# Kernel optimization log

Hardware: AMD Instinct MI355X
Metric: run time of the kernel (lower is better)

The kernel has to match this reference:

```python
import jax, jax.numpy as jnp
import numpy as np

KH = KW = 3
STRIDE = 1
ITERATIONS = 2
EPS = 1e-7


def _squash(s):
    # squash along last axis (capsule dim)
    sn = jnp.sum(s * s, axis=-1, keepdims=True)
    return (sn / (1.0 + sn)) * s / jnp.sqrt(sn + EPS)


def setup_inputs() -> dict:
    key = jax.random.key(0)
    k1, k2 = jax.random.split(key)
    x = jax.random.normal(k1, (4, 14, 14, 32, 8), dtype=jnp.float32)
    # W: [1,1,1,filters_out, caps_per_patch=3*3*32, dims_out=16, dims_in=8], stddev=0.1 init
    W = 0.1 * jax.random.normal(k2, (1, 1, 1, 32, 288, 16, 8), dtype=jnp.float32)
    return {"x": x, "W": W}


def reference(x, W):
    B, H, Wd, Fin, Din = x.shape
    Ho = (H - KH) // STRIDE + 1
    Wo = (Wd - KW) // STRIDE + 1
    # Patch extraction, channel order (kh, kw, Fin) to match tf.image.extract_patches
    patches = jnp.stack(
        [x[:, i:i + Ho * STRIDE:STRIDE, j:j + Wo * STRIDE:STRIDE]
         for i in range(KH) for j in range(KW)],
        axis=3,
    )  # [B,Ho,Wo,KH*KW,Fin,Din]
    patches = patches.reshape(B, Ho, Wo, KH * KW * Fin, Din)  # [B,Ho,Wo,C,Di]

    Wm = W[0, 0, 0]  # [F, C, Do, Di]
    F, C, Do, _ = Wm.shape
    # predictions[b,h,w,f,c,o] = sum_i W[f,c,o,i] * patches[b,h,w,c,i]
    preds = jnp.einsum('fcoi,bhwci->bhwfco', Wm, patches)

    logits = jnp.zeros((B, Ho, Wo, F, C), dtype=preds.dtype)
    outputs = jnp.zeros((B, Ho, Wo, F, Do), dtype=preds.dtype)
    for _ in range(ITERATIONS):
        # agreement = predictions^T @ outputs over the dims_out axis
        agreement = jnp.einsum('bhwfco,bhwfo->bhwfc', preds, outputs)
        logits = logits + agreement
        # NOTE: original code softmaxes over axis=3 (the filters_out axis)
        cc = jax.nn.softmax(logits, axis=3)  # [B,Ho,Wo,F,C]
        centroids = jnp.sum(cc[..., None] * preds, axis=4)  # [B,Ho,Wo,F,Do]
        outputs = _squash(centroids)
    return outputs
```

## Files before the change

kernel.cpp:

```cpp
#include <hip/hip_runtime.h>

#define NB   4
#define H_IN 14
#define W_IN 14
#define FIN  32
#define DI   8
#define F    32
#define C    288
#define DO   16
#define HO   12
#define WO   12
#define NPOS (NB*HO*WO)
#define EPS  1e-7f

#define CH   16
#define CC   (C/CH)
#define GP   8
#define GRID (CH*(NPOS/GP))

#define KTOT (C*DI)
#define KPAD 2312

#define W2H_BYTES  ((size_t)F*C*DO*DI*2)
#define WH_BYTES   ((size_t)F*C*DO*DI*2)
#define PH_BYTES   ((size_t)NPOS*KTOT*2)
#define PART_BYTES ((size_t)CH*NPOS*F*DO*4)
#define OUT1_BYTES ((size_t)NPOS*F*DO*4)

#define CVT_W2H 576
#define CVT_WH  576
#define CVT_PH  648
#define CVT_GRID (CVT_W2H + CVT_WH + CVT_PH)

typedef _Float16 h2 __attribute__((ext_vector_type(2)));
typedef _Float16 h8v __attribute__((ext_vector_type(8)));
typedef float    f4v __attribute__((ext_vector_type(4)));

__device__ __forceinline__ unsigned int pack2(float a, float b) {
    h2 v; v.x = (_Float16)a; v.y = (_Float16)b;
    return __builtin_bit_cast(unsigned int, v);
}

__device__ __forceinline__ float dot8h(const uint4 w, const uint4 v, float acc) {
#if __has_builtin(__builtin_amdgcn_fdot2)
    acc = __builtin_amdgcn_fdot2(__builtin_bit_cast(h2, w.x), __builtin_bit_cast(h2, v.x), acc, false);
    acc = __builtin_amdgcn_fdot2(__builtin_bit_cast(h2, w.y), __builtin_bit_cast(h2, v.y), acc, false);
    acc = __builtin_amdgcn_fdot2(__builtin_bit_cast(h2, w.z), __builtin_bit_cast(h2, v.z), acc, false);
    acc = __builtin_amdgcn_fdot2(__builtin_bit_cast(h2, w.w), __builtin_bit_cast(h2, v.w), acc, false);
#else
    const h2 w0 = __builtin_bit_cast(h2, w.x), v0 = __builtin_bit_cast(h2, v.x);
    const h2 w1 = __builtin_bit_cast(h2, w.y), v1 = __builtin_bit_cast(h2, v.y);
    const h2 w2 = __builtin_bit_cast(h2, w.z), v2 = __builtin_bit_cast(h2, v.z);
    const h2 w3 = __builtin_bit_cast(h2, w.w), v3 = __builtin_bit_cast(h2, v.w);
    acc += (float)w0.x*(float)v0.x + (float)w0.y*(float)v0.y
         + (float)w1.x*(float)v1.x + (float)w1.y*(float)v1.y
         + (float)w2.x*(float)v2.x + (float)w2.y*(float)v2.y
         + (float)w3.x*(float)v3.x + (float)w3.y*(float)v3.y;
#endif
    return acc;
}

__device__ __forceinline__ int xbase_of(int pos) {
    const int b = pos/(HO*WO), rem = pos%(HO*WO), ho = rem/WO, wo = rem%WO;
    return ((b*H_IN + ho)*W_IN + wo)*FIN*DI;
}

__device__ __forceinline__ int coff_of(int c) {
    const int slab = c >> 5, fin = c & 31;
    const int kh = slab/3, kw = slab%3;
    return (kh*W_IN + kw)*FIN*DI + fin*DI;
}

__global__ __launch_bounds__(256) void kernConv(const float* __restrict__ Wt,
                                                const float* __restrict__ x,
                                                unsigned short* __restrict__ W2h,
                                                unsigned short* __restrict__ Wh,
                                                unsigned short* __restrict__ Ph) {
    const int b = blockIdx.x;
    if (b < CVT_W2H) {
        const int idx = b*256 + threadIdx.x;
        const float* src = Wt + (size_t)idx*8;
        const float4 a = *(const float4*)src;
        const float4 bb = *(const float4*)(src + 4);
        uint4 r;
        r.x = pack2(a.x, a.y);   r.y = pack2(a.z, a.w);
        r.z = pack2(bb.x, bb.y); r.w = pack2(bb.z, bb.w);
        const int o = idx & 15;
        const int c = (idx >> 4) % C;
        const int f = idx / (C*DO);
        ((uint4*)W2h)[(size_t)(c*DO + o)*F + f] = r;
    } else if (b < CVT_W2H + CVT_WH) {
        const int idx = (b - CVT_W2H)*256 + threadIdx.x;
        const float* src = Wt + (size_t)idx*8;
        const float4 a = *(const float4*)src;
        const float4 bb = *(const float4*)(src + 4);
        uint4 r;
        r.x = pack2(a.x, a.y);   r.y = pack2(a.z, a.w);
        r.z = pack2(bb.x, bb.y); r.w = pack2(bb.z, bb.w);
        ((uint4*)Wh)[idx] = r;
    } else {
        const int pc = (b - CVT_W2H - CVT_WH)*256 + threadIdx.x;
        const int pos = pc / C, c = pc % C;
        const float* src = x + xbase_of(pos) + coff_of(c);
        const float4 a = *(const float4*)src;
        const float4 bb = *(const float4*)(src + 4);
        uint4 r;
        r.x = pack2(a.x, a.y);   r.y = pack2(a.z, a.w);
        r.z = pack2(bb.x, bb.y); r.w = pack2(bb.z, bb.w);
        ((uint4*)Ph)[pc] = r;
    }
}

__global__ __launch_bounds__(256) void kernM1(const unsigned short* __restrict__ Ph,
                                              const unsigned short* __restrict__ Wh,
                                              float* __restrict__ out1)
{
    __shared__ unsigned short As[16][KPAD];

    const int tid  = threadIdx.x;
    const int lane = tid & 63;
    const int wv   = tid >> 6;
    const int pt   = blockIdx.x >> 3;
    const int fg   = blockIdx.x & 7;
    const int f    = wv*8 + fg;
    const int pos0 = pt*16;
    const int n    = lane & 15, q = lane >> 4;

    #pragma unroll
    for (int r = 0; r < 18; ++r) {
        const int linear = r*256 + tid;
        const int row = linear / 288, col8 = linear % 288;
        const uint4 v = *(const uint4*)(Ph + (size_t)(pos0 + row)*KTOT + col8*8);
        *(uint4*)&As[row][col8*8] = v;
    }
    __syncthreads();

    const unsigned short* pa = &As[n][q*8];
    const unsigned short* pb = Wh + ((size_t)(f*C + q)*DO + n)*DI;

    f4v acc0 = {0.f,0.f,0.f,0.f}, acc1 = {0.f,0.f,0.f,0.f};
    #pragma unroll 4
    for (int s = 0; s < KTOT/32; s += 2) {
        const h8v a0 = *(const h8v*)(pa + s*32);
        const h8v b0 = *(const h8v*)(pb + (size_t)s*4*DO*DI);
        const h8v a1 = *(const h8v*)(pa + (s+1)*32);
        const h8v b1 = *(const h8v*)(pb + (size_t)(s+1)*4*DO*DI);
        acc0 = __builtin_amdgcn_mfma_f32_16x16x32_f16(a0, b0, acc0, 0, 0, 0);
        acc1 = __builtin_amdgcn_mfma_f32_16x16x32_f16(a1, b1, acc1, 0, 0, 0);
    }

    #pragma unroll
    for (int r = 0; r < 4; ++r) {
        const float v = (acc0[r] + acc1[r]) * (1.f/32.f);
        float sq = v*v;
        sq += __shfl_xor(sq, 1);
        sq += __shfl_xor(sq, 2);
        sq += __shfl_xor(sq, 4);
        sq += __shfl_xor(sq, 8);
        const float sc = (sq/(1.f + sq)) * rsqrtf(sq + EPS);
        out1[(size_t)(pos0 + q*4 + r)*512 + f*DO + n] = v * sc;
    }
}

__global__ __launch_bounds__(256) void kern2n(const unsigned short* __restrict__ Ph,
                                              const unsigned short* __restrict__ W2h,
                                              const float* __restrict__ out1,
                                              float* __restrict__ part2)
{
    __shared__ float red[2][4][GP][32];
    __shared__ float ccs[2][GP][32];

    const int tid = threadIdx.x;
    const int f  = tid & 31;
    const int og = tid >> 5;
    const int o0 = 2*og, o1 = o0 + 1;
    const int wv = tid >> 6;
    const int half = (tid >> 5) & 1;
    const int ch = blockIdx.x & (CH-1);
    const int pg = blockIdx.x >> 4;

    int poff[GP];
    #pragma unroll
    for (int p = 0; p < GP; ++p) poff[p] = (pg*GP + p)*KTOT;

    float u0[GP], u1[GP];
    #pragma unroll
    for (int p = 0; p < GP; ++p) {
        const float* up = out1 + (size_t)(pg*GP + p)*512 + f*DO;
        u0[p] = up[o0];
        u1[p] = up[o1];
    }

    const uint4* W2h4 = (const uint4*)W2h;
    const int c0 = ch*CC;

    float acc0[GP], acc1[GP];
    #pragma unroll
    for (int p = 0; p < GP; ++p) { acc0[p] = 0.f; acc1[p] = 0.f; }

    #pragma unroll 1
    for (int cl = 0; cl < CC; ++cl) {
        const int c = c0 + cl;
        const int buf = cl & 1;
        const uint4 w0 = W2h4[(size_t)(c*DO + o0)*F + f];
        const uint4 w1 = W2h4[(size_t)(c*DO + o1)*F + f];

        float pred0[GP], pred1[GP];
        #pragma unroll
        for (int p = 0; p < GP; ++p) {
            const uint4 xv = *(const uint4*)(Ph + poff[p] + c*DI);
            pred0[p] = dot8h(w0, xv, 0.f);
            pred1[p] = dot8h(w1, xv, 0.f);
        }

        #pragma unroll
        for (int p = 0; p < GP; ++p) {
            float ap = pred0[p]*u0[p] + pred1[p]*u1[p];
            ap += __shfl_xor(ap, 32);
            if (half == 0) red[buf][wv][p][f] = ap;
        }
        __syncthreads();

        {
            const int p2 = tid >> 5, f2 = tid & 31;
            const float agr = red[buf][0][p2][f2] + red[buf][1][p2][f2]
                            + red[buf][2][p2][f2] + red[buf][3][p2][f2];
            float m = agr;
            m = fmaxf(m, __shfl_xor(m, 1));
            m = fmaxf(m, __shfl_xor(m, 2));
            m = fmaxf(m, __shfl_xor(m, 4));
            m = fmaxf(m, __shfl_xor(m, 8));
            m = fmaxf(m, __shfl_xor(m, 16));
            const float e = __expf(agr - m);
            float s = e;
            s += __shfl_xor(s, 1);
            s += __shfl_xor(s, 2);
            s += __shfl_xor(s, 4);
            s += __shfl_xor(s, 8);
            s += __shfl_xor(s, 16);
            ccs[buf][p2][f2] = e / s;
        }
        __syncthreads();

        #pragma unroll
        for (int p = 0; p < GP; ++p) {
            const float cv = ccs[buf][p][f];
            acc0[p] += cv*pred0[p];
            acc1[p] += cv*pred1[p];
        }
    }

    #pragma unroll
    for (int p = 0; p < GP; ++p) {
        const size_t base = ((size_t)(ch*NPOS + pg*GP + p))*DO;
        part2[(base + o0)*F + f] = acc0[p];
        part2[(base + o1)*F + f] = acc1[p];
    }
}

__global__ __launch_bounds__(256) void kern3(const float* __restrict__ part2,
                                             float* __restrict__ out)
{
    const int tid = threadIdx.x;
    const int f = tid & 31, p = tid >> 5;
    const int pos = blockIdx.x*8 + p;

    float cent[DO];
    #pragma unroll
    for (int o = 0; o < DO; ++o) cent[o] = 0.f;
    #pragma unroll 1
    for (int k = 0; k < CH; ++k) {
        const float* s = part2 + (size_t)(k*NPOS + pos)*512 + f;
        #pragma unroll
        for (int o = 0; o < DO; ++o) cent[o] += s[o*F];
    }
    float sn = 0.f;
    #pragma unroll
    for (int o = 0; o < DO; ++o) sn += cent[o]*cent[o];
    const float sc = (sn/(1.f + sn)) * rsqrtf(sn + EPS);
    float* dst = out + ((size_t)pos*F + f)*DO;
    #pragma unroll
    for (int o = 0; o < DO; ++o) dst[o] = cent[o]*sc;
}

__device__ __forceinline__ float dot8(const float4* __restrict__ w,
                                      const float4 p0, const float4 p1) {
    float4 a = w[0], b = w[1];
    return a.x*p0.x + a.y*p0.y + a.z*p0.z + a.w*p0.w
         + b.x*p1.x + b.y*p1.y + b.z*p1.z + b.w*p1.w;
}

__global__ __launch_bounds__(256) void capsule_kernel_f32(
    const float* __restrict__ x, const float* __restrict__ Wt,
    float* __restrict__ out)
{
    __shared__ float patch[C*DI];
    __shared__ float cent[F*DO];
    __shared__ float out1[F*DO];
    __shared__ float agr[F*C];
    __shared__ float scale_s[F];

    const int tid = threadIdx.x;
    const int pos = blockIdx.x;
    const int b   = pos / (HO*WO);
    const int rem = pos % (HO*WO);
    const int ho  = rem / WO;
    const int wo  = rem % WO;

    #pragma unroll
    for (int slab = 0; slab < 9; ++slab) {
        const int kh = slab / 3, kw = slab % 3;
        const float* src = x + (((b*H_IN + ho + kh)*W_IN + (wo + kw))*FIN)*DI;
        patch[slab*256 + tid] = src[tid];
    }
    __syncthreads();

    const float4* pv = (const float4*)patch;

    {
        const int fo0 = tid, fo1 = tid + 256;
        const int f0 = fo0 >> 4, o0 = fo0 & 15;
        const int f1 = fo1 >> 4, o1 = fo1 & 15;
        float acc0 = 0.f, acc1 = 0.f;
        for (int c = 0; c < C; ++c) {
            const float4 p0 = pv[c*2], p1 = pv[c*2+1];
            acc0 += dot8((const float4*)(Wt + ((f0*C + c)*DO + o0)*DI), p0, p1);
            acc1 += dot8((const float4*)(Wt + ((f1*C + c)*DO + o1)*DI), p0, p1);
        }
        cent[fo0] = acc0 * (1.f/32.f);
        cent[fo1] = acc1 * (1.f/32.f);
    }
    __syncthreads();

    if (tid < F) {
        float sn = 0.f;
        #pragma unroll
        for (int o = 0; o < DO; ++o) { float v = cent[tid*DO + o]; sn += v*v; }
        const float sc = (sn/(1.f + sn)) * rsqrtf(sn + EPS);
        #pragma unroll
        for (int o = 0; o < DO; ++o) out1[tid*DO + o] = cent[tid*DO + o] * sc;
    }
    __syncthreads();

    #pragma unroll 1
    for (int r = 0; r < (F*C)/256; ++r) {
        const int pp = tid + 256*r;
        const int f = pp / C, c = pp % C;
        const float4* wrow = (const float4*)(Wt + (f*C + c)*DO*DI);
        const float4 p0 = pv[c*2], p1 = pv[c*2+1];
        float a = 0.f;
        #pragma unroll
        for (int o = 0; o < DO; ++o) a += dot8(wrow + o*2, p0, p1) * out1[f*DO + o];
        agr[pp] = a;
    }
    __syncthreads();

    for (int c = tid; c < C; c += 256) {
        float m = -1e30f;
        #pragma unroll
        for (int f = 0; f < F; ++f) m = fmaxf(m, agr[f*C + c]);
        float s = 0.f;
        #pragma unroll
        for (int f = 0; f < F; ++f) {
            const float e = __expf(agr[f*C + c] - m);
            agr[f*C + c] = e; s += e;
        }
        const float inv = 1.f / s;
        #pragma unroll
        for (int f = 0; f < F; ++f) agr[f*C + c] *= inv;
    }
    __syncthreads();

    {
        const int fo0 = tid, fo1 = tid + 256;
        const int f0 = fo0 >> 4, o0 = fo0 & 15;
        const int f1 = fo1 >> 4, o1 = fo1 & 15;
        float acc0 = 0.f, acc1 = 0.f;
        for (int c = 0; c < C; ++c) {
            const float4 p0 = pv[c*2], p1 = pv[c*2+1];
            acc0 += agr[f0*C + c] * dot8((const float4*)(Wt + ((f0*C + c)*DO + o0)*DI), p0, p1);
            acc1 += agr[f1*C + c] * dot8((const float4*)(Wt + ((f1*C + c)*DO + o1)*DI), p0, p1);
        }
        cent[fo0] = acc0;
        cent[fo1] = acc1;
    }
    __syncthreads();

    if (tid < F) {
        float sn = 0.f;
        #pragma unroll
        for (int o = 0; o < DO; ++o) { float v = cent[tid*DO + o]; sn += v*v; }
        scale_s[tid] = (sn/(1.f + sn)) * rsqrtf(sn + EPS);
    }
    __syncthreads();

    out[pos*(F*DO) + tid]       = cent[tid]       * scale_s[tid >> 4];
    out[pos*(F*DO) + tid + 256] = cent[tid + 256] * scale_s[(tid >> 4) + 16];
}

extern "C" void kernel_launch(void* const* d_in, const int* in_sizes, int n_in,
                              void* d_out, int out_size, void* d_ws, size_t ws_size,
                              hipStream_t stream) {
    const float* x  = (const float*)d_in[0];
    const float* Wt = (const float*)d_in[1];
    float* out = (float*)d_out;

    if (ws_size >= W2H_BYTES + WH_BYTES + PH_BYTES + PART_BYTES + OUT1_BYTES) {
        char* p = (char*)d_ws;
        unsigned short* W2h = (unsigned short*)p;            p += W2H_BYTES;
        unsigned short* Wh  = (unsigned short*)p;            p += WH_BYTES;
        unsigned short* Ph  = (unsigned short*)p;            p += PH_BYTES;
        float* part = (float*)p;                             p += PART_BYTES;
        float* out1 = (float*)p;

        kernConv<<<CVT_GRID, 256, 0, stream>>>(Wt, x, W2h, Wh, Ph);
        kernM1<<<36*8, 256, 0, stream>>>(Ph, Wh, out1);
        kern2n<<<GRID, 256, 0, stream>>>(Ph, W2h, out1, part);
        kern3<<<NPOS/8, 256, 0, stream>>>(part, out);
    } else {
        capsule_kernel_f32<<<NPOS, 256, 0, stream>>>(x, Wt, out);
    }
}
```

Measured before the change: 133.5 us.

## Process two capsules per iteration and store fp16 partial centroids

```diff
diff --git a/kernel.cpp b/kernel.cpp
--- a/kernel.cpp
+++ b/kernel.cpp
@@ -24,7 +24,7 @@
 #define W2H_BYTES  ((size_t)F*C*DO*DI*2)
 #define WH_BYTES   ((size_t)F*C*DO*DI*2)
 #define PH_BYTES   ((size_t)NPOS*KTOT*2)
-#define PART_BYTES ((size_t)CH*NPOS*F*DO*4)
+#define PART_BYTES ((size_t)CH*NPOS*F*DO*2)
 #define OUT1_BYTES ((size_t)NPOS*F*DO*4)
 
 #define CVT_W2H 576
@@ -165,7 +165,7 @@
 __global__ __launch_bounds__(256) void kern2n(const unsigned short* __restrict__ Ph,
                                               const unsigned short* __restrict__ W2h,
                                               const float* __restrict__ out1,
-                                              float* __restrict__ part2)
+                                              unsigned short* __restrict__ part2h)
 {
     __shared__ float red[2][4][GP][32];
     __shared__ float ccs[2][GP][32];
@@ -199,66 +199,78 @@
     for (int p = 0; p < GP; ++p) { acc0[p] = 0.f; acc1[p] = 0.f; }
 
     #pragma unroll 1
-    for (int cl = 0; cl < CC; ++cl) {
-        const int c = c0 + cl;
-        const int buf = cl & 1;
-        const uint4 w0 = W2h4[(size_t)(c*DO + o0)*F + f];
-        const uint4 w1 = W2h4[(size_t)(c*DO + o1)*F + f];
-
-        float pred0[GP], pred1[GP];
+    for (int cp = 0; cp < CC/2; ++cp) {
+        const int ca = c0 + cp*2, cb = ca + 1;
+        const uint4 wa0 = W2h4[(size_t)(ca*DO + o0)*F + f];
+        const uint4 wa1 = W2h4[(size_t)(ca*DO + o1)*F + f];
+        const uint4 wb0 = W2h4[(size_t)(cb*DO + o0)*F + f];
+        const uint4 wb1 = W2h4[(size_t)(cb*DO + o1)*F + f];
+
+        float pa0[GP], pa1[GP], pb0[GP], pb1[GP];
         #pragma unroll
         for (int p = 0; p < GP; ++p) {
-            const uint4 xv = *(const uint4*)(Ph + poff[p] + c*DI);
-            pred0[p] = dot8h(w0, xv, 0.f);
-            pred1[p] = dot8h(w1, xv, 0.f);
+            const uint4 xa = *(const uint4*)(Ph + poff[p] + ca*DI);
+            const uint4 xb = *(const uint4*)(Ph + poff[p] + cb*DI);
+            pa0[p] = dot8h(wa0, xa, 0.f);
+            pa1[p] = dot8h(wa1, xa, 0.f);
+            pb0[p] = dot8h(wb0, xb, 0.f);
+            pb1[p] = dot8h(wb1, xb, 0.f);
         }
 
         #pragma unroll
         for (int p = 0; p < GP; ++p) {
-            float ap = pred0[p]*u0[p] + pred1[p]*u1[p];
-            ap += __shfl_xor(ap, 32);
-            if (half == 0) red[buf][wv][p][f] = ap;
+            float apa = pa0[p]*u0[p] + pa1[p]*u1[p];
+            float apb = pb0[p]*u0[p] + pb1[p]*u1[p];
+            apa += __shfl_xor(apa, 32);
+            apb += __shfl_xor(apb, 32);
+            if (half == 0) {
+                red[0][wv][p][f] = apa;
+                red[1][wv][p][f] = apb;
+            }
         }
         __syncthreads();
 
         {
             const int p2 = tid >> 5, f2 = tid & 31;
-            const float agr = red[buf][0][p2][f2] + red[buf][1][p2][f2]
-                            + red[buf][2][p2][f2] + red[buf][3][p2][f2];
-            float m = agr;
-            m = fmaxf(m, __shfl_xor(m, 1));
-            m = fmaxf(m, __shfl_xor(m, 2));
-            m = fmaxf(m, __shfl_xor(m, 4));
-            m = fmaxf(m, __shfl_xor(m, 8));
-            m = fmaxf(m, __shfl_xor(m, 16));
-            const float e = __expf(agr - m);
-            float s = e;
-            s += __shfl_xor(s, 1);
-            s += __shfl_xor(s, 2);
-            s += __shfl_xor(s, 4);
-            s += __shfl_xor(s, 8);
-            s += __shfl_xor(s, 16);
-            ccs[buf][p2][f2] = e / s;
+            #pragma unroll
+            for (int sub = 0; sub < 2; ++sub) {
+                const float agr = red[sub][0][p2][f2] + red[sub][1][p2][f2]
+                                + red[sub][2][p2][f2] + red[sub][3][p2][f2];
+                float m = agr;
+                m = fmaxf(m, __shfl_xor(m, 1));
+                m = fmaxf(m, __shfl_xor(m, 2));
+                m = fmaxf(m, __shfl_xor(m, 4));
+                m = fmaxf(m, __shfl_xor(m, 8));
+                m = fmaxf(m, __shfl_xor(m, 16));
+                const float e = __expf(agr - m);
+                float s = e;
+                s += __shfl_xor(s, 1);
+                s += __shfl_xor(s, 2);
+                s += __shfl_xor(s, 4);
+                s += __shfl_xor(s, 8);
+                s += __shfl_xor(s, 16);
+                ccs[sub][p2][f2] = e / s;
+            }
         }
         __syncthreads();
 
         #pragma unroll
         for (int p = 0; p < GP; ++p) {
-            const float cv = ccs[buf][p][f];
-            acc0[p] += cv*pred0[p];
-            acc1[p] += cv*pred1[p];
+            const float cva = ccs[0][p][f];
+            const float cvb = ccs[1][p][f];
+            acc0[p] += cva*pa0[p] + cvb*pb0[p];
+            acc1[p] += cva*pa1[p] + cvb*pb1[p];
         }
     }
 
     #pragma unroll
     for (int p = 0; p < GP; ++p) {
-        const size_t base = ((size_t)(ch*NPOS + pg*GP + p))*DO;
-        part2[(base + o0)*F + f] = acc0[p];
-        part2[(base + o1)*F + f] = acc1[p];
-    }
-}
-
-__global__ __launch_bounds__(256) void kern3(const float* __restrict__ part2,
+        const size_t base = ((size_t)(ch*NPOS + pg*GP + p)*F + f)*DO;
+        ((unsigned int*)(part2h + base))[og] = pack2(acc0[p], acc1[p]);
+    }
+}
+
+__global__ __launch_bounds__(256) void kern3(const unsigned short* __restrict__ part2h,
                                              float* __restrict__ out)
 {
     const int tid = threadIdx.x;
@@ -270,17 +282,25 @@
     for (int o = 0; o < DO; ++o) cent[o] = 0.f;
     #pragma unroll 1
     for (int k = 0; k < CH; ++k) {
-        const float* s = part2 + (size_t)(k*NPOS + pos)*512 + f;
-        #pragma unroll
-        for (int o = 0; o < DO; ++o) cent[o] += s[o*F];
+        const uint4* s = (const uint4*)(part2h + ((size_t)(k*NPOS + pos)*F + f)*DO);
+        const uint4 v0 = s[0], v1 = s[1];
+        const unsigned int w[8] = {v0.x, v0.y, v0.z, v0.w, v1.x, v1.y, v1.z, v1.w};
+        #pragma unroll
+        for (int q = 0; q < 8; ++q) {
+            const h2 hv = __builtin_bit_cast(h2, w[q]);
+            cent[2*q]   += (float)hv.x;
+            cent[2*q+1] += (float)hv.y;
+        }
     }
     float sn = 0.f;
     #pragma unroll
     for (int o = 0; o < DO; ++o) sn += cent[o]*cent[o];
     const float sc = (sn/(1.f + sn)) * rsqrtf(sn + EPS);
-    float* dst = out + ((size_t)pos*F + f)*DO;
-    #pragma unroll
-    for (int o = 0; o < DO; ++o) dst[o] = cent[o]*sc;
+    float4* dst = (float4*)(out + ((size_t)pos*F + f)*DO);
+    dst[0] = make_float4(cent[0]*sc,  cent[1]*sc,  cent[2]*sc,  cent[3]*sc);
+    dst[1] = make_float4(cent[4]*sc,  cent[5]*sc,  cent[6]*sc,  cent[7]*sc);
+    dst[2] = make_float4(cent[8]*sc,  cent[9]*sc,  cent[10]*sc, cent[11]*sc);
+    dst[3] = make_float4(cent[12]*sc, cent[13]*sc, cent[14]*sc, cent[15]*sc);
 }
 
 __device__ __forceinline__ float dot8(const float4* __restrict__ w,
@@ -410,13 +430,13 @@
         unsigned short* W2h = (unsigned short*)p;            p += W2H_BYTES;
         unsigned short* Wh  = (unsigned short*)p;            p += WH_BYTES;
         unsigned short* Ph  = (unsigned short*)p;            p += PH_BYTES;
-        float* part = (float*)p;                             p += PART_BYTES;
+        unsigned short* part2h = (unsigned short*)p;         p += PART_BYTES;
         float* out1 = (float*)p;
 
         kernConv<<<CVT_GRID, 256, 0, stream>>>(Wt, x, W2h, Wh, Ph);
         kernM1<<<36*8, 256, 0, stream>>>(Ph, Wh, out1);
-        kern2n<<<GRID, 256, 0, stream>>>(Ph, W2h, out1, part);
-        kern3<<<NPOS/8, 256, 0, stream>>>(part, out);
+        kern2n<<<GRID, 256, 0, stream>>>(Ph, W2h, out1, part2h);
+        kern3<<<NPOS/8, 256, 0, stream>>>(part2h, out);
     } else {
         capsule_kernel_f32<<<NPOS, 256, 0, stream>>>(x, Wt, out);
     }
```

Result: no change. 136.1 us (+1.9%).
